# Kernel tuning notes

Measured on AMD Instinct MI355X. Metric: run time of the kernel, lower is better.

Reference implementation:

```python
import jax, jax.numpy as jnp
import numpy as np

N = [100000, 25000, 6250]        # nodes per scale (coarsening pyramid)
F = 128                          # features_per_scale (all equal)
H = 4                            # num_heads (only enters via the score scale)
SCALE = float((F // H) ** 0.5)
OUT = 5                          # out_channels
E_SAME = [1000000, 400000, 100000]
E_INC = [400000, 100000]


def _cross_attn(src, dst, src_feat, n_dst, qW, qb, kW, kb, vW, vb):
    # GAT-style gather -> per-edge score -> segment softmax over dst -> scatter.
    # In the original model dst_feat is zeros, so Q = 0 @ qW + qb; we keep the
    # matmul so qW appears in the autodiff graph (its grad is zero, faithfully).
    K = src_feat @ kW + kb
    V = src_feat @ vW + vb
    Q = jnp.zeros((n_dst, qW.shape[1]), src_feat.dtype) @ qW + qb
    score = (Q[dst] * K[src]).sum(-1) / SCALE            # [E]
    m = jax.ops.segment_max(score, dst, num_segments=n_dst)
    e = jnp.exp(score - m[dst])
    denom = jax.ops.segment_sum(e, dst, num_segments=n_dst)
    attn = e / denom[dst]                                # segment softmax
    return jax.ops.segment_sum(attn[:, None] * V[src], dst, num_segments=n_dst)


def _gcn(src, dst, x, n, W, b):
    # DGL GraphConv, norm='both': D_out^-1/2 -> scatter-sum -> D_in^-1/2 -> linear.
    ones = jnp.ones(src.shape[0], x.dtype)
    deg_out = jnp.clip(jax.ops.segment_sum(ones, src, num_segments=n), 1.0)
    deg_in = jnp.clip(jax.ops.segment_sum(ones, dst, num_segments=n), 1.0)
    h = x * jax.lax.rsqrt(deg_out)[:, None]
    agg = jax.ops.segment_sum(h[src], dst, num_segments=n)
    return (agg * jax.lax.rsqrt(deg_in)[:, None]) @ W + b


def setup_inputs() -> dict:
    key = jax.random.key(0)
    cnt = [0]
    def rkey():
        cnt[0] += 1
        return jax.random.fold_in(key, cnt[0])
    def rn(shape, s=0.05):
        return jax.random.normal(rkey(), shape, jnp.float32) * s
    def ri(n, hi):
        return jax.random.randint(rkey(), (n,), 0, hi, jnp.int32)
    return {
        "X": rn((N[0], F), 1.0),
        "emb_W": rn((F, F)), "emb_b": rn((F,)),
        "gcn_W": rn((3, F, F)), "gcn_b": rn((3, F)),
        "enc_qW": rn((2, F, F)), "enc_qb": rn((2, F)),
        "enc_kW": rn((2, F, F)), "enc_kb": rn((2, F)),
        "enc_vW": rn((2, F, F)), "enc_vb": rn((2, F)),
        "dec_qW": rn((2, F, F)), "dec_qb": rn((2, F)),
        "dec_kW": rn((2, F, F)), "dec_kb": rn((2, F)),
        "dec_vW": rn((2, F, F)), "dec_vb": rn((2, F)),
        "head_W": rn((3, 2 * F, OUT)), "head_b": rn((3, OUT)),
        "g0_src": ri(E_SAME[0], N[0]), "g0_dst": ri(E_SAME[0], N[0]),
        "g1_src": ri(E_SAME[1], N[1]), "g1_dst": ri(E_SAME[1], N[1]),
        "g2_src": ri(E_SAME[2], N[2]), "g2_dst": ri(E_SAME[2], N[2]),
        "inc0_src": ri(E_INC[0], N[0]), "inc0_dst": ri(E_INC[0], N[1]),
        "inc1_src": ri(E_INC[1], N[1]), "inc1_dst": ri(E_INC[1], N[2]),
        "dec0_src": ri(E_INC[1], N[2]), "dec0_dst": ri(E_INC[1], N[1]),
        "dec1_src": ri(E_INC[0], N[1]), "dec1_dst": ri(E_INC[0], N[0]),
    }


def reference(X, emb_W, emb_b, gcn_W, gcn_b,
              enc_qW, enc_qb, enc_kW, enc_kb, enc_vW, enc_vb,
              dec_qW, dec_qb, dec_kW, dec_kb, dec_vW, dec_vb,
              head_W, head_b,
              g0_src, g0_dst, g1_src, g1_dst, g2_src, g2_dst,
              inc0_src, inc0_dst, inc1_src, inc1_dst,
              dec0_src, dec0_dst, dec1_src, dec1_dst):
    h0 = X @ emb_W + emb_b                               # embedding, scale 0
    # encoder: scale 0 -> 1 -> 2
    e1 = _cross_attn(inc0_src, inc0_dst, h0, N[1],
                     enc_qW[0], enc_qb[0], enc_kW[0], enc_kb[0], enc_vW[0], enc_vb[0])
    e2 = _cross_attn(inc1_src, inc1_dst, e1, N[2],
                     enc_qW[1], enc_qb[1], enc_kW[1], enc_kb[1], enc_vW[1], enc_vb[1])
    feats = [h0, e1, e2]
    edges = [(g0_src, g0_dst), (g1_src, g1_dst), (g2_src, g2_dst)]
    gcn_out = [_gcn(s, d, feats[i], N[i], gcn_W[i], gcn_b[i])
               for i, (s, d) in enumerate(edges)]
    # decoder: scale 2 -> 1 -> 0
    d1 = _cross_attn(dec0_src, dec0_dst, gcn_out[2], N[1],
                     dec_qW[0], dec_qb[0], dec_kW[0], dec_kb[0], dec_vW[0], dec_vb[0])
    d0 = _cross_attn(dec1_src, dec1_dst, d1, N[0],
                     dec_qW[1], dec_qb[1], dec_kW[1], dec_kb[1], dec_vW[1], dec_vb[1])
    decoded = [d0, d1, gcn_out[2]]
    outs = [jax.nn.softmax(jnp.concatenate([gcn_out[i], decoded[i]], -1) @ head_W[i] + head_b[i], -1)
            for i in range(3)]
    return jnp.concatenate(outs, 0)                      # [N0+N1+N2, OUT]
```

## Files before the change

### kernel.cpp

```cpp
#include <hip/hip_runtime.h>
#include <math.h>

#define N0 100000
#define N1 25000
#define N2 6250
#define FD 128

typedef unsigned short u16;
typedef unsigned int u32;

static inline int ceildiv(int a, int b){ return (a + b - 1)/b; }

__device__ __forceinline__ u16 f2bf(float f){
  u32 u = __float_as_uint(f);
  u += 0x7fffu + ((u >> 16) & 1u);
  return (u16)(u >> 16);
}
__device__ __forceinline__ float bf2f(u16 h){
  return __uint_as_float(((u32)h) << 16);
}
__device__ __forceinline__ float blo(u32 u){ return __uint_as_float(u << 16); }
__device__ __forceinline__ float bhi(u32 u){ return __uint_as_float(u & 0xffff0000u); }
__device__ __forceinline__ u32 pk2(float a, float b){ return (u32)f2bf(a) | ((u32)f2bf(b) << 16); }

struct BMeta {
  const int* key[10];
  const int* src[7];
  int* rowp[7]; int* csr[7];
  float* rsout[3];
  int n[10], E[10], B[10], r[10];
  int eoff[8];
  int soff[4];
  int boff[11];
  int pblk[11];
};

__device__ __forceinline__ void mm_inner(const float* Al, const float* Wl, int r0, int c0, float acc[4][4]){
  #pragma unroll
  for (int kq = 0; kq < 8; ++kq) {
    int k0 = kq*4;
    float4 a[4], w[4];
    #pragma unroll
    for (int i=0;i<4;++i) a[i] = *(const float4*)&Al[(r0+i)*32 + k0];
    #pragma unroll
    for (int kk=0;kk<4;++kk) w[kk] = *(const float4*)&Wl[(k0+kk)*128 + c0];
    #pragma unroll
    for (int i=0;i<4;++i){
      acc[i][0] = fmaf(a[i].x,w[0].x, fmaf(a[i].y,w[1].x, fmaf(a[i].z,w[2].x, fmaf(a[i].w,w[3].x, acc[i][0]))));
      acc[i][1] = fmaf(a[i].x,w[0].y, fmaf(a[i].y,w[1].y, fmaf(a[i].z,w[2].y, fmaf(a[i].w,w[3].y, acc[i][1]))));
      acc[i][2] = fmaf(a[i].x,w[0].z, fmaf(a[i].y,w[1].z, fmaf(a[i].z,w[2].z, fmaf(a[i].w,w[3].z, acc[i][2]))));
      acc[i][3] = fmaf(a[i].x,w[0].w, fmaf(a[i].y,w[1].w, fmaf(a[i].z,w[2].w, fmaf(a[i].w,w[3].w, acc[i][3]))));
    }
  }
}

template<int SCORE, int AB16>
__device__ __forceinline__ void dev_gemm(float* Wl, float* Al, int bid,
    const void* __restrict__ Ap,
    const float* __restrict__ W, const float* __restrict__ bias,
    const float* __restrict__ kvec, float* __restrict__ sOut,
    u16* __restrict__ out, int n)
{
  const int tid = threadIdx.x;
  const int row0 = bid * 32;
  const int c0 = (tid & 31) * 4, r0 = (tid >> 5) * 4;
  const int r = tid >> 3, fc = tid & 7;
  const int gr_s = row0 + r;
  float acc[4][4] = {};
  float sacc = 0.f;
  const float4* W4 = (const float4*)W;
  for (int kp = 0; kp < 4; ++kp) {
    float4* Wl4 = (float4*)Wl;
    #pragma unroll
    for (int i = 0; i < 4; ++i) Wl4[tid + 256*i] = W4[kp*1024 + tid + 256*i];
    {
      float4 v = make_float4(0.f,0.f,0.f,0.f);
      if (gr_s < n){
        if (AB16){
          ushort4 h = ((const ushort4*)Ap)[(size_t)gr_s*32 + kp*8 + fc];
          v = make_float4(bf2f(h.x), bf2f(h.y), bf2f(h.z), bf2f(h.w));
        } else {
          v = ((const float4*)Ap)[(size_t)gr_s*32 + kp*8 + fc];
        }
      }
      ((float4*)Al)[tid] = v;
      if (SCORE){
        float4 kv = *(const float4*)&kvec[kp*32 + fc*4];
        sacc += v.x*kv.x + v.y*kv.y + v.z*kv.z + v.w*kv.w;
      }
    }
    __syncthreads();
    mm_inner(Al, Wl, r0, c0, acc);
    __syncthreads();
  }
  if (SCORE){
    sacc += __shfl_xor(sacc, 1);
    sacc += __shfl_xor(sacc, 2);
    sacc += __shfl_xor(sacc, 4);
    if (fc == 0 && gr_s < n) sOut[gr_s] = expf(sacc + kvec[128]);
  }
  float4 bv = make_float4(0.f,0.f,0.f,0.f);
  if (bias) bv = *(const float4*)&bias[c0];
  #pragma unroll
  for (int i=0;i<4;++i){
    int gr = row0 + r0 + i;
    if (gr < n){
      ushort4 o;
      o.x = f2bf(acc[i][0]+bv.x); o.y = f2bf(acc[i][1]+bv.y);
      o.z = f2bf(acc[i][2]+bv.z); o.w = f2bf(acc[i][3]+bv.w);
      *(ushort4*)&out[(size_t)gr*FD + c0] = o;
    }
  }
}

template<int AB16>
__device__ __forceinline__ void dev_dualgemm(float* sm, int bid,
    const void* __restrict__ Ap,
    const float* __restrict__ Wv, const float* __restrict__ vb,
    const float* __restrict__ Wg,
    const float* __restrict__ kvec, float* __restrict__ sOut,
    u16* __restrict__ Vout, u16* __restrict__ Yout, int n)
{
  float* WvL = sm; float* WgL = sm + 4096; float* Al = sm + 8192;
  const int tid = threadIdx.x;
  const int row0 = bid * 32;
  const int c0 = (tid & 31) * 4, r0 = (tid >> 5) * 4;
  const int r = tid >> 3, fc = tid & 7;
  const int gr_s = row0 + r;
  float accV[4][4] = {};
  float accY[4][4] = {};
  float sacc = 0.f;
  const float4* Wv4 = (const float4*)Wv;
  const float4* Wg4 = (const float4*)Wg;
  for (int kp = 0; kp < 4; ++kp) {
    #pragma unroll
    for (int i = 0; i < 4; ++i) ((float4*)WvL)[tid + 256*i] = Wv4[kp*1024 + tid + 256*i];
    #pragma unroll
    for (int i = 0; i < 4; ++i) ((float4*)WgL)[tid + 256*i] = Wg4[kp*1024 + tid + 256*i];
    {
      float4 v = make_float4(0.f,0.f,0.f,0.f);
      if (gr_s < n){
        if (AB16){
          ushort4 h = ((const ushort4*)Ap)[(size_t)gr_s*32 + kp*8 + fc];
          v = make_float4(bf2f(h.x), bf2f(h.y), bf2f(h.z), bf2f(h.w));
        } else {
          v = ((const float4*)Ap)[(size_t)gr_s*32 + kp*8 + fc];
        }
      }
      ((float4*)Al)[tid] = v;
      float4 kv = *(const float4*)&kvec[kp*32 + fc*4];
      sacc += v.x*kv.x + v.y*kv.y + v.z*kv.z + v.w*kv.w;
    }
    __syncthreads();
    mm_inner(Al, WvL, r0, c0, accV);
    mm_inner(Al, WgL, r0, c0, accY);
    __syncthreads();
  }
  sacc += __shfl_xor(sacc, 1);
  sacc += __shfl_xor(sacc, 2);
  sacc += __shfl_xor(sacc, 4);
  if (fc == 0 && gr_s < n) sOut[gr_s] = expf(sacc + kvec[128]);
  float4 bv = *(const float4*)&vb[c0];
  #pragma unroll
  for (int i=0;i<4;++i){
    int gr = row0 + r0 + i;
    if (gr < n){
      ushort4 o;
      o.x = f2bf(accV[i][0]+bv.x); o.y = f2bf(accV[i][1]+bv.y);
      o.z = f2bf(accV[i][2]+bv.z); o.w = f2bf(accV[i][3]+bv.w);
      *(ushort4*)&Vout[(size_t)gr*FD + c0] = o;
      ushort4 y;
      y.x = f2bf(accY[i][0]); y.y = f2bf(accY[i][1]);
      y.z = f2bf(accY[i][2]); y.w = f2bf(accY[i][3]);
      *(ushort4*)&Yout[(size_t)gr*FD + c0] = y;
    }
  }
}

__device__ __forceinline__ int job_of_blk(const BMeta& m, int bid){
  int j = 0;
  #pragma unroll
  for (int t = 1; t < 10; ++t) if (bid >= m.pblk[t]) j = t;
  return j;
}

__device__ __forceinline__ void dev_p0(const BMeta& m, int bid, int* __restrict__ bktCnt, int* sh){
  int j = job_of_blk(m, bid);
  int lb = bid - m.pblk[j];
  const int* key = m.key[j]; int E = m.E[j], r = m.r[j], B = m.B[j];
  if (threadIdx.x < 64) sh[threadIdx.x] = 0;
  __syncthreads();
  int base = lb*4096 + threadIdx.x;
  #pragma unroll
  for (int i = 0; i < 16; ++i){ int e = base + i*256; if (e < E) atomicAdd(&sh[key[e]/r], 1); }
  __syncthreads();
  if ((int)threadIdx.x < B) atomicAdd(&bktCnt[m.boff[j] + threadIdx.x], sh[threadIdx.x]);
}

__device__ __forceinline__ void dev_p1(const BMeta& m, const int* __restrict__ bktCnt,
    int* __restrict__ bktBase, int* __restrict__ bktCur, int* sh){
  int tid = threadIdx.x;
  for (int i = tid; i < 328; i += 256) sh[i] = bktCnt[i];
  __syncthreads();
  if (tid < 10){
    int acc = (tid < 7) ? m.eoff[tid] : m.soff[tid-7];
    for (int b = m.boff[tid]; b < m.boff[tid+1]; ++b){ int v = sh[b]; sh[b] = acc; acc += v; }
  }
  __syncthreads();
  for (int i = tid; i < 328; i += 256){ bktBase[i] = sh[i]; bktCur[i] = sh[i]; }
}

__device__ __forceinline__ void dev_p2(const BMeta& m, int bid, int* __restrict__ bktCur,
    u32* __restrict__ ebuf, u16* __restrict__ ebuf16, int* sh){
  int j = job_of_blk(m, bid);
  int lb = bid - m.pblk[j];
  const int* key = m.key[j];
  int E = m.E[j], r = m.r[j], B = m.B[j];
  int* h = sh; int* start = sh + 64;
  if (threadIdx.x < 64) h[threadIdx.x] = 0;
  __syncthreads();
  int base = lb*4096 + threadIdx.x;
  #pragma unroll
  for (int i = 0; i < 16; ++i){ int e = base + i*256; if (e < E) atomicAdd(&h[key[e]/r], 1); }
  __syncthreads();
  if ((int)threadIdx.x < B) start[threadIdx.x] = atomicAdd(&bktCur[m.boff[j] + threadIdx.x], h[threadIdx.x]);
  __syncthreads();
  if (j < 7){
    const int* src = m.src[j];
    #pragma unroll
    for (int i = 0; i < 16; ++i){
      int e = base + i*256;
      if (e < E){
        int s = src[e], d = key[e];
        int b = d / r;
        int pos = atomicAdd(&start[b], 1);
        ebuf[pos] = ((u32)(d - b*r) << 17) | (u32)s;
      }
    }
  } else {
    #pragma unroll
    for (int i = 0; i < 16; ++i){
      int e = base + i*256;
      if (e < E){
        int k = key[e];
        int b = k / r;
        int pos = atomicAdd(&start[b], 1);
        ebuf16[pos] = (u16)(k - b*r);
      }
    }
  }
}

__device__ __forceinline__ void dev_p3(const BMeta& m, int bb,
    const int* __restrict__ bktCnt, const int* __restrict__ bktBase,
    const u32* __restrict__ ebuf, const u16* __restrict__ ebuf16, int* sh){
  int j = 0;
  #pragma unroll
  for (int t = 1; t < 10; ++t) if (bb >= m.boff[t]) j = t;
  int b = bb - m.boff[j];
  int n = m.n[j], r = m.r[j];
  int node0 = b*r;
  int rr = min(r, n - node0);
  int gbase = bktBase[bb];
  int cnt = bktCnt[bb];
  int tid = threadIdx.x;
  if (j >= 7){
    int* hist = sh;
    for (int i = tid; i < rr; i += 256) hist[i] = 0;
    __syncthreads();
    for (int e = tid; e < cnt; e += 256) atomicAdd(&hist[ebuf16[gbase + e]], 1);
    __syncthreads();
    float* rs = m.rsout[j-7];
    for (int i = tid; i < rr; i += 256) rs[node0 + i] = rsqrtf(fmaxf((float)hist[i], 1.f));
    return;
  }
  int B = m.B[j];
  int* rowp = m.rowp[j]; int* csr = m.csr[j];
  int lbase = gbase - m.eoff[j];
  int* hist = sh; int* aux = sh + 1568;
  for (int i = tid; i < rr; i += 256) hist[i] = 0;
  __syncthreads();
  for (int e = tid; e < cnt; e += 256){ u32 pk = ebuf[gbase + e]; atomicAdd(&hist[pk >> 17], 1); }
  __syncthreads();
  int ch = (rr + 255) >> 8;
  int i0 = tid*ch;
  int s = 0;
  for (int k = 0; k < ch; ++k){ int idx = i0 + k; if (idx < rr){ int t = hist[idx]; hist[idx] = s; s += t; } }
  aux[tid] = s; __syncthreads();
  for (int off = 1; off < 256; off <<= 1){
    int v = aux[tid]; int a = (tid >= off) ? aux[tid - off] : 0;
    __syncthreads();
    aux[tid] = v + a;
    __syncthreads();
  }
  int pre = (tid ? aux[tid-1] : 0) + lbase;
  for (int k = 0; k < ch; ++k){ int idx = i0 + k; if (idx < rr) hist[idx] += pre; }
  __syncthreads();
  for (int i = tid; i < rr; i += 256) rowp[node0 + i] = hist[i];
  if (b == B-1 && tid == 0) rowp[n] = lbase + cnt;
  __syncthreads();
  for (int e = tid; e < cnt; e += 256){
    u32 pk = ebuf[gbase + e];
    int pos = atomicAdd(&hist[pk >> 17], 1);
    csr[pos] = (int)(pk & 0x1FFFFu);
  }
}

template<int OB16>
__device__ __forceinline__ void dev_attn_gather16(int bid,
    const int* __restrict__ csr, const int* __restrict__ rowp,
    const float* __restrict__ w, const u16* __restrict__ V,
    void* __restrict__ out, int n)
{
  int g = threadIdx.x >> 4, lane = threadIdx.x & 15;
  int row = bid*16 + g;
  if (row >= n) return;
  int st = rowp[row], en = rowp[row+1];
  float a0=0,a1=0,a2=0,a3=0,a4=0,a5=0,a6=0,a7=0;
  if (en > st){
    const uint4* V8 = (const uint4*)V;
    float den = 0.f;
    for (int e = st; e < en; ++e){
      int sn = csr[e];
      float x = w[sn];
      uint4 v = V8[(size_t)sn*16 + lane];
      den += x;
      a0 = fmaf(x, blo(v.x), a0); a1 = fmaf(x, bhi(v.x), a1);
      a2 = fmaf(x, blo(v.y), a2); a3 = fmaf(x, bhi(v.y), a3);
      a4 = fmaf(x, blo(v.z), a4); a5 = fmaf(x, bhi(v.z), a5);
      a6 = fmaf(x, blo(v.w), a6); a7 = fmaf(x, bhi(v.w), a7);
    }
    float inv = 1.f/den;
    a0*=inv; a1*=inv; a2*=inv; a3*=inv; a4*=inv; a5*=inv; a6*=inv; a7*=inv;
  }
  if (OB16){
    uint4 o; o.x = pk2(a0,a1); o.y = pk2(a2,a3); o.z = pk2(a4,a5); o.w = pk2(a6,a7);
    ((uint4*)out)[(size_t)row*16 + lane] = o;
  } else {
    float4* o4 = (float4*)out;
    o4[(size_t)row*32 + lane*2]     = make_float4(a0,a1,a2,a3);
    o4[(size_t)row*32 + lane*2 + 1] = make_float4(a4,a5,a6,a7);
  }
}

template<int OB16>
__device__ __forceinline__ void dev_gcn_gather16(int bid,
    const int* __restrict__ csr, const int* __restrict__ rowp,
    const float* __restrict__ rs, const u16* __restrict__ Y,
    const float* __restrict__ bias, void* __restrict__ out, int n)
{
  int g = threadIdx.x >> 4, lane = threadIdx.x & 15;
  int row = bid*16 + g;
  if (row >= n) return;
  int st = rowp[row], en = rowp[row+1];
  float a0=0,a1=0,a2=0,a3=0,a4=0,a5=0,a6=0,a7=0;
  const uint4* Y8 = (const uint4*)Y;
  for (int e = st; e < en; ++e){
    int sn = csr[e];
    float x = rs[sn];
    uint4 v = Y8[(size_t)sn*16 + lane];
    a0 = fmaf(x, blo(v.x), a0); a1 = fmaf(x, bhi(v.x), a1);
    a2 = fmaf(x, blo(v.y), a2); a3 = fmaf(x, bhi(v.y), a3);
    a4 = fmaf(x, blo(v.z), a4); a5 = fmaf(x, bhi(v.z), a5);
    a6 = fmaf(x, blo(v.w), a6); a7 = fmaf(x, bhi(v.w), a7);
  }
  float sc = rsqrtf(fmaxf((float)(en - st), 1.f));
  const float4* b4 = (const float4*)bias;
  float4 ba = b4[lane*2], bb = b4[lane*2+1];
  float o0=fmaf(a0,sc,ba.x), o1=fmaf(a1,sc,ba.y), o2=fmaf(a2,sc,ba.z), o3=fmaf(a3,sc,ba.w);
  float o4v=fmaf(a4,sc,bb.x), o5=fmaf(a5,sc,bb.y), o6=fmaf(a6,sc,bb.z), o7=fmaf(a7,sc,bb.w);
  if (OB16){
    uint4 o; o.x = pk2(o0,o1); o.y = pk2(o2,o3); o.z = pk2(o4v,o5); o.w = pk2(o6,o7);
    ((uint4*)out)[(size_t)row*16 + lane] = o;
  } else {
    float4* o4 = (float4*)out;
    o4[(size_t)row*32 + lane*2]     = make_float4(o0,o1,o2,o3);
    o4[(size_t)row*32 + lane*2 + 1] = make_float4(o4v,o5,o6,o7);
  }
}

template<int GB16, int DB16>
__device__ __forceinline__ void dev_head(int bid, const void* __restrict__ g, const void* __restrict__ dch,
    const float* __restrict__ W, const float* __restrict__ b,
    float* __restrict__ out, int n, int rowOff)
{
  int wid = threadIdx.x >> 6, lane = threadIdx.x & 63;
  int row = bid*4 + wid;
  if (row >= n) return;
  float x0, x1, x2, x3;
  if (GB16){ const u16* gr = (const u16*)g + (size_t)row*FD; x0 = bf2f(gr[lane]); x1 = bf2f(gr[64+lane]); }
  else     { const float* gr = (const float*)g + (size_t)row*FD; x0 = gr[lane]; x1 = gr[64+lane]; }
  if (DB16){ const u16* dr = (const u16*)dch + (size_t)row*FD; x2 = bf2f(dr[lane]); x3 = bf2f(dr[64+lane]); }
  else     { const float* dr = (const float*)dch + (size_t)row*FD; x2 = dr[lane]; x3 = dr[64+lane]; }
  float acc[5];
  #pragma unroll
  for (int o = 0; o < 5; ++o)
    acc[o] = x0*W[lane*5+o] + x1*W[(64+lane)*5+o] + x2*W[(128+lane)*5+o] + x3*W[(192+lane)*5+o];
  #pragma unroll
  for (int o = 0; o < 5; ++o)
    #pragma unroll
    for (int s = 32; s; s >>= 1) acc[o] += __shfl_xor(acc[o], s);
  if (lane == 0){
    float m = -1e30f;
    #pragma unroll
    for (int o = 0; o < 5; ++o){ acc[o] += b[o]; m = fmaxf(m, acc[o]); }
    float sum = 0.f;
    #pragma unroll
    for (int o = 0; o < 5; ++o){ acc[o] = expf(acc[o]-m); sum += acc[o]; }
    float is = 1.0f/sum;
    float* op = out + (size_t)(rowOff+row)*5;
    #pragma unroll
    for (int o = 0; o < 5; ++o) op[o] = acc[o]*is;
  }
}


__global__ __launch_bounds__(256) void k1_zero_kqv(int* __restrict__ zeroBlk, int ntot,
    const float* __restrict__ ekW, const float* __restrict__ ekb, const float* __restrict__ eqb,
    const float* __restrict__ dkW, const float* __restrict__ dkb, const float* __restrict__ dqb,
    float* __restrict__ kv, float inv)
{
  int bid = blockIdx.x;
  if (bid < 4){
    if (threadIdx.x < 128){
      int j = bid;
      const float* kW = (j < 2) ? ekW + j*16384 : dkW + (j-2)*16384;
      const float* kb = (j < 2) ? ekb + j*128   : dkb + (j-2)*128;
      const float* qb = (j < 2) ? eqb + j*128   : dqb + (j-2)*128;
      float* o = kv + j*132;
      int k = threadIdx.x;
      float a = 0.f;
      for (int t = 0; t < 128; ++t) a = fmaf(kW[k*128+t], qb[t], a);
      o[k] = a * inv;
      if (k == 0){
        float c = 0.f;
        for (int t = 0; t < 128; ++t) c = fmaf(kb[t], qb[t], c);
        o[128] = c * inv;
      }
    }
  } else {
    int i = (bid-4)*256 + threadIdx.x;
    if (i < ntot) zeroBlk[i] = 0;
  }
}

__global__ __launch_bounds__(256) void k2_p0_gemm(BMeta m, int* __restrict__ bktCnt,
    const float* __restrict__ X, const float* __restrict__ W, const float* __restrict__ b,
    u16* __restrict__ bh0, int np0)
{
  __shared__ float sm[5120];
  int bid = blockIdx.x;
  if (bid < np0) dev_p0(m, bid, bktCnt, (int*)sm);
  else dev_gemm<0,0>(sm, sm+4096, bid - np0, X, W, b, nullptr, nullptr, bh0, N0);
}

__global__ __launch_bounds__(256) void k3_p1(BMeta m,
    const int* __restrict__ bktCnt, int* __restrict__ bktBase, int* __restrict__ bktCur)
{
  __shared__ int sh[384];
  dev_p1(m, bktCnt, bktBase, bktCur, sh);
}

__global__ __launch_bounds__(256) void k4_p2_dual(BMeta m, int* __restrict__ bktCur,
    u32* __restrict__ ebuf, u16* __restrict__ ebuf16,
    const u16* __restrict__ bh0,
    const float* __restrict__ evW, const float* __restrict__ evb, const float* __restrict__ gW,
    const float* __restrict__ kvec, float* __restrict__ sS, u16* __restrict__ bV, u16* __restrict__ bY0,
    int np2, int gOff)
{
  __shared__ float sm[9216];
  int bid = blockIdx.x;
  if (bid < np2) dev_p2(m, bid, bktCur, ebuf, ebuf16, (int*)sm);
  else dev_dualgemm<1>(sm, gOff + bid - np2, bh0, evW, evb, gW, kvec, sS, bV, bY0, N0);
}

__global__ __launch_bounds__(256) void k5_p3_dual(BMeta m,
    const int* __restrict__ bktCnt, const int* __restrict__ bktBase,
    const u32* __restrict__ ebuf, const u16* __restrict__ ebuf16,
    const u16* __restrict__ bh0,
    const float* __restrict__ evW, const float* __restrict__ evb, const float* __restrict__ gW,
    const float* __restrict__ kvec, float* __restrict__ sS, u16* __restrict__ bV, u16* __restrict__ bY0,
    int np3, int gOff)
{
  __shared__ float sm[9216];
  int bid = blockIdx.x;
  if (bid < np3) dev_p3(m, bid, bktCnt, bktBase, ebuf, ebuf16, (int*)sm);
  else dev_dualgemm<1>(sm, gOff + bid - np3, bh0, evW, evb, gW, kvec, sS, bV, bY0, N0);
}

__global__ __launch_bounds__(256) void k6_ag_i0(
    const int* __restrict__ csrA, const int* __restrict__ rowpA,
    const float* __restrict__ sS, const u16* __restrict__ bV, u16* __restrict__ be1,
    const int* __restrict__ csr0, const int* __restrict__ rowp0, const float* __restrict__ rs0,
    const u16* __restrict__ bY0, const float* __restrict__ gb, u16* __restrict__ bg0, int nMain, int sBase)
{
  int bid = blockIdx.x;
  if (bid < nMain) dev_attn_gather16<1>(bid, csrA, rowpA, sS, bV, be1, N1);
  else dev_gcn_gather16<1>(sBase + bid - nMain, csr0, rowp0, rs0, bY0, gb, bg0, N0);
}

__global__ __launch_bounds__(256) void k7_dual_enc1(
    const u16* __restrict__ be1,
    const float* __restrict__ vW, const float* __restrict__ vb, const float* __restrict__ gW,
    const float* __restrict__ kvec, float* __restrict__ sS, u16* __restrict__ bV, u16* __restrict__ bY1,
    const int* __restrict__ csr0, const int* __restrict__ rowp0, const float* __restrict__ rs0,
    const u16* __restrict__ bY0, const float* __restrict__ gb, u16* __restrict__ bg0, int nMain, int sBase)
{
  __shared__ float sm[9216];
  int bid = blockIdx.x;
  if (bid < nMain) dev_dualgemm<1>(sm, bid, be1, vW, vb, gW, kvec, sS, bV, bY1, N1);
  else dev_gcn_gather16<1>(sBase + bid - nMain, csr0, rowp0, rs0, bY0, gb, bg0, N0);
}

__global__ __launch_bounds__(256) void k8_ag_i1(
    const int* __restrict__ csrA, const int* __restrict__ rowpA,
    const float* __restrict__ sS, const u16* __restrict__ bV, float* __restrict__ be2,
    const int* __restrict__ csr0, const int* __restrict__ rowp0, const float* __restrict__ rs0,
    const u16* __restrict__ bY0, const float* __restrict__ gb, u16* __restrict__ bg0, int nMain, int sBase)
{
  int bid = blockIdx.x;
  if (bid < nMain) dev_attn_gather16<0>(bid, csrA, rowpA, sS, bV, be2, N2);
  else dev_gcn_gather16<1>(sBase + bid - nMain, csr0, rowp0, rs0, bY0, gb, bg0, N0);
}

__global__ __launch_bounds__(256) void k9_y2_g1(
    const float* __restrict__ be2, const float* __restrict__ W2, u16* __restrict__ bY2,
    const int* __restrict__ csr1, const int* __restrict__ rowp1, const float* __restrict__ rs1,
    const u16* __restrict__ bY1, const float* __restrict__ b1, u16* __restrict__ bg1,
    const int* __restrict__ csr0, const int* __restrict__ rowp0, const float* __restrict__ rs0,
    const u16* __restrict__ bY0, const float* __restrict__ gb, u16* __restrict__ bg0,
    int ngemm, int nMain, int sBase)
{
  __shared__ float sm[5120];
  int bid = blockIdx.x;
  if (bid < ngemm) dev_gemm<0,0>(sm, sm+4096, bid, be2, W2, nullptr, nullptr, nullptr, bY2, N2);
  else if (bid < nMain) dev_gcn_gather16<1>(bid - ngemm, csr1, rowp1, rs1, bY1, b1, bg1, N1);
  else dev_gcn_gather16<1>(sBase + bid - nMain, csr0, rowp0, rs0, bY0, gb, bg0, N0);
}

__global__ __launch_bounds__(256) void k10_g2(
    const int* __restrict__ csr2, const int* __restrict__ rowp2, const float* __restrict__ rs2,
    const u16* __restrict__ bY2, const float* __restrict__ b2, float* __restrict__ bg2,
    const int* __restrict__ csr0, const int* __restrict__ rowp0, const float* __restrict__ rs0,
    const u16* __restrict__ bY0, const float* __restrict__ gb, u16* __restrict__ bg0, int nMain, int sBase)
{
  int bid = blockIdx.x;
  if (bid < nMain) dev_gcn_gather16<0>(bid, csr2, rowp2, rs2, bY2, b2, bg2, N2);
  else dev_gcn_gather16<1>(sBase + bid - nMain, csr0, rowp0, rs0, bY0, gb, bg0, N0);
}

__global__ __launch_bounds__(256) void k11_dec0_head2(
    const float* __restrict__ bg2, const float* __restrict__ vW, const float* __restrict__ vb,
    const float* __restrict__ kvec, float* __restrict__ sS, u16* __restrict__ bV,
    const float* __restrict__ hW, const float* __restrict__ hb, float* __restrict__ out,
    const int* __restrict__ csr0, const int* __restrict__ rowp0, const float* __restrict__ rs0,
    const u16* __restrict__ bY0, const float* __restrict__ gb, u16* __restrict__ bg0,
    int ngemm, int nMain, int sBase)
{
  __shared__ float sm[5120];
  int bid = blockIdx.x;
  if (bid < ngemm) dev_gemm<1,0>(sm, sm+4096, bid, bg2, vW, vb, kvec, sS, bV, N2);
  else if (bid < nMain) dev_head<0,0>(bid - ngemm, bg2, bg2, hW, hb, out, N2, N0+N1);
  else dev_gcn_gather16<1>(sBase + bid - nMain, csr0, rowp0, rs0, bY0, gb, bg0, N0);
}

__global__ __launch_bounds__(256) void k12_ag_d1(
    const int* __restrict__ csrA, const int* __restrict__ rowpA,
    const float* __restrict__ sS, const u16* __restrict__ bV, u16* __restrict__ be1,
    const int* __restrict__ csr0, const int* __restrict__ rowp0, const float* __restrict__ rs0,
    const u16* __restrict__ bY0, const float* __restrict__ gb, u16* __restrict__ bg0, int nMain, int sBase)
{
  int bid = blockIdx.x;
  if (bid < nMain) dev_attn_gather16<1>(bid, csrA, rowpA, sS, bV, be1, N1);
  else dev_gcn_gather16<1>(sBase + bid - nMain, csr0, rowp0, rs0, bY0, gb, bg0, N0);
}

__global__ __launch_bounds__(256) void k13_dec1_head1(
    const u16* __restrict__ be1, const float* __restrict__ vW, const float* __restrict__ vb,
    const float* __restrict__ kvec, float* __restrict__ sS, u16* __restrict__ bV,
    const u16* __restrict__ bg1, const float* __restrict__ hW, const float* __restrict__ hb,
    float* __restrict__ out,
    const int* __restrict__ csr0, const int* __restrict__ rowp0, const float* __restrict__ rs0,
    const u16* __restrict__ bY0, const float* __restrict__ gb, u16* __restrict__ bg0,
    int ngemm, int nMain, int sBase)
{
  __shared__ float sm[5120];
  int bid = blockIdx.x;
  if (bid < ngemm) dev_gemm<1,1>(sm, sm+4096, bid, be1, vW, vb, kvec, sS, bV, N1);
  else if (bid < nMain) dev_head<1,1>(bid - ngemm, bg1, be1, hW, hb, out, N1, N0);
  else dev_gcn_gather16<1>(sBase + bid - nMain, csr0, rowp0, rs0, bY0, gb, bg0, N0);
}

__global__ __launch_bounds__(256) void k14_gather_head0(
    const int* __restrict__ csr, const int* __restrict__ rowp,
    const float* __restrict__ w, const u16* __restrict__ V,
    const u16* __restrict__ bg0,
    const float* __restrict__ hW, const float* __restrict__ hb,
    float* __restrict__ out)
{
  int g = threadIdx.x >> 4, lane = threadIdx.x & 15;
  int row = blockIdx.x*16 + g;
  if (row >= N0) return;
  int st = rowp[row], en = rowp[row+1];
  float a0=0,a1=0,a2=0,a3=0,a4=0,a5=0,a6=0,a7=0;
  if (en > st){
    const uint4* V8 = (const uint4*)V;
    float den = 0.f;
    for (int e = st; e < en; ++e){
      int sn = csr[e];
      float x = w[sn];
      uint4 v = V8[(size_t)sn*16 + lane];
      den += x;
      a0 = fmaf(x, blo(v.x), a0); a1 = fmaf(x, bhi(v.x), a1);
      a2 = fmaf(x, blo(v.y), a2); a3 = fmaf(x, bhi(v.y), a3);
      a4 = fmaf(x, blo(v.z), a4); a5 = fmaf(x, bhi(v.z), a5);
      a6 = fmaf(x, blo(v.w), a6); a7 = fmaf(x, bhi(v.w), a7);
    }
    float inv = 1.f/den;
    a0*=inv; a1*=inv; a2*=inv; a3*=inv; a4*=inv; a5*=inv; a6*=inv; a7*=inv;
  }
  uint4 gv = ((const uint4*)(bg0 + (size_t)row*FD))[lane];
  float g0 = blo(gv.x), g1 = bhi(gv.x), g2 = blo(gv.y), g3 = bhi(gv.y);
  float g4 = blo(gv.z), g5 = bhi(gv.z), g6 = blo(gv.w), g7 = bhi(gv.w);
  int j = 8*lane;
  float acc[5];
  #pragma unroll
  for (int o = 0; o < 5; ++o){
    acc[o] = g0*hW[(j+0)*5+o] + g1*hW[(j+1)*5+o] + g2*hW[(j+2)*5+o] + g3*hW[(j+3)*5+o]
           + g4*hW[(j+4)*5+o] + g5*hW[(j+5)*5+o] + g6*hW[(j+6)*5+o] + g7*hW[(j+7)*5+o]
           + a0*hW[(128+j+0)*5+o] + a1*hW[(128+j+1)*5+o] + a2*hW[(128+j+2)*5+o] + a3*hW[(128+j+3)*5+o]
           + a4*hW[(128+j+4)*5+o] + a5*hW[(128+j+5)*5+o] + a6*hW[(128+j+6)*5+o] + a7*hW[(128+j+7)*5+o];
  }
  #pragma unroll
  for (int o = 0; o < 5; ++o)
    #pragma unroll
    for (int s = 8; s; s >>= 1) acc[o] += __shfl_xor(acc[o], s, 16);
  if (lane == 0){
    float m = -1e30f;
    #pragma unroll
    for (int o = 0; o < 5; ++o){ acc[o] += hb[o]; m = fmaxf(m, acc[o]); }
    float sum = 0.f;
    #pragma unroll
    for (int o = 0; o < 5; ++o){ acc[o] = expf(acc[o]-m); sum += acc[o]; }
    float is = 1.0f/sum;
    float* op = out + (size_t)row*5;
    #pragma unroll
    for (int o = 0; o < 5; ++o) op[o] = acc[o]*is;
  }
}

extern "C" void kernel_launch(void* const* d_in, const int* in_sizes, int n_in,
                              void* d_out, int out_size, void* d_ws, size_t ws_size,
                              hipStream_t stream)
{
  const float* X      = (const float*)d_in[0];
  const float* emb_W  = (const float*)d_in[1];
  const float* emb_b  = (const float*)d_in[2];
  const float* gcn_W  = (const float*)d_in[3];
  const float* gcn_b  = (const float*)d_in[4];
  const float* enc_qb = (const float*)d_in[6];
  const float* enc_kW = (const float*)d_in[7];
  const float* enc_kb = (const float*)d_in[8];
  const float* enc_vW = (const float*)d_in[9];
  const float* enc_vb = (const float*)d_in[10];
  const float* dec_qb = (const float*)d_in[12];
  const float* dec_kW = (const float*)d_in[13];
  const float* dec_kb = (const float*)d_in[14];
  const float* dec_vW = (const float*)d_in[15];
  const float* dec_vb = (const float*)d_in[16];
  const float* head_W = (const float*)d_in[17];
  const float* head_b = (const float*)d_in[18];
  const int* g0s  = (const int*)d_in[19];
  const int* g0d  = (const int*)d_in[20];
  const int* g1s  = (const int*)d_in[21];
  const int* g1d  = (const int*)d_in[22];
  const int* g2s  = (const int*)d_in[23];
  const int* g2d  = (const int*)d_in[24];
  const int* i0s  = (const int*)d_in[25];
  const int* i0d  = (const int*)d_in[26];
  const int* i1s  = (const int*)d_in[27];
  const int* i1d  = (const int*)d_in[28];
  const int* dc0s = (const int*)d_in[29];
  const int* dc0d = (const int*)d_in[30];
  const int* dc1s = (const int*)d_in[31];
  const int* dc1d = (const int*)d_in[32];

  float* ws = (float*)d_ws;
  float* sS  = ws;
  float* kvec = sS + N0;
  float* be2 = kvec + 4*132;
  float* bg2 = be2 + (size_t)N2*FD;
  float* rs0 = bg2 + (size_t)N2*FD;
  float* rs1 = rs0 + N0;
  float* rs2 = rs1 + N1;
  u16*  bh0 = (u16*)(rs2 + N2 + 2);
  u16*  be1 = bh0 + (size_t)N0*FD;
  u16*  bg0 = be1 + (size_t)N1*FD;
  u16*  bg1 = bg0 + (size_t)N0*FD;
  u16*  bV  = bg1 + (size_t)N1*FD;
  u16*  bY0 = bV  + (size_t)N0*FD;
  u16*  bY1 = bV + 4000000;
  u16*  bY2 = bV + 8000000;
  int*  bktCnt  = (int*)(bY0 + (size_t)N0*FD);
  int*  bktBase = bktCnt + 328;
  int*  bktCur  = bktBase + 328;
  int*  rowpBlk = bktCur + 328;
  int*  csrBlk  = rowpBlk + 287507;
  u32*  ebuf    = (u32*)(csrBlk + 2500000);
  u16*  ebuf16  = (u16*)(ebuf + 2500000);

  const int* keyP[10] = {g0d,g1d,g2d,i0d,i1d,dc0d,dc1d, g0s,g1s,g2s};
  const int* srcP[7]  = {g0s,g1s,g2s,i0s,i1s,dc0s,dc1s};
  const int nArr[10] = {N0,N1,N2,N1,N2,N1,N0, N0,N1,N2};
  const int EArr[10] = {1000000,400000,100000,400000,100000,100000,400000, 1000000,400000,100000};
  const int BArr[10] = {64,32,8,32,8,16,64, 64,32,8};
  const int rArr[10] = {1563,782,782,782,782,1563,1563, 1563,782,782};

  BMeta m;
  {
    int eo=0, so=0, bo=0, po=0, ro=0, co=0;
    for (int j=0;j<10;++j){
      m.key[j]=keyP[j];
      m.n[j]=nArr[j]; m.E[j]=EArr[j]; m.B[j]=BArr[j]; m.r[j]=rArr[j];
      m.boff[j]=bo; m.pblk[j]=po;
      bo+=BArr[j]; po+=ceildiv(EArr[j],4096);
      if (j < 7){
        m.src[j]=srcP[j]; m.rowp[j]=rowpBlk+ro; m.csr[j]=csrBlk+co;
        m.eoff[j]=eo; eo+=EArr[j]; ro+=nArr[j]+1; co+=EArr[j];
      } else {
        m.soff[j-7]=so; so+=EArr[j];
      }
    }
    m.eoff[7]=eo; m.soff[3]=so; m.boff[10]=bo; m.pblk[10]=po;
  }
  m.rsout[0]=rs0; m.rsout[1]=rs1; m.rsout[2]=rs2;

  const float invScale = 0.17677669529663687f;
  float* out = (float*)d_out;

  const int NP = m.pblk[10];
  const int NB = m.boff[10];
  const int GH0 = ceildiv(N0,32);
  const int GH1 = ceildiv(N1,32);
  const int GH2 = ceildiv(N2,32);
  const int GS1 = 1250;
  const int GA1_16 = ceildiv(N1,16);
  const int GA2_16 = ceildiv(N2,16);
  const int G0B16  = ceildiv(N0,16);
  const int GH2H = ceildiv(N2,4);
  const int GH1H = ceildiv(N1,4);

  int ss[9];
  for (int i = 0; i <= 8; ++i) ss[i] = (int)(((long long)G0B16 * i) / 8);

  k1_zero_kqv<<<4 + ceildiv(NB,256), 256, 0, stream>>>(bktCnt, NB,
      enc_kW, enc_kb, enc_qb, dec_kW, dec_kb, dec_qb, kvec, invScale);
  k2_p0_gemm<<<NP + GH0, 256, 0, stream>>>(m, bktCnt, X, emb_W, emb_b, bh0, NP);
  k3_p1<<<1, 256, 0, stream>>>(m, bktCnt, bktBase, bktCur);
  k4_p2_dual<<<NP + GS1, 256, 0, stream>>>(m, bktCur, ebuf, ebuf16,
      bh0, enc_vW, enc_vb, gcn_W, kvec, sS, bV, bY0, NP, 0);
  k5_p3_dual<<<NB + (GH0 - GS1), 256, 0, stream>>>(m, bktCnt, bktBase, ebuf, ebuf16,
      bh0, enc_vW, enc_vb, gcn_W, kvec, sS, bV, bY0, NB, GS1);
  k6_ag_i0<<<GA1_16 + (ss[1]-ss[0]), 256, 0, stream>>>(m.csr[3], m.rowp[3], sS, bV, be1,
      m.csr[0], m.rowp[0], rs0, bY0, gcn_b, bg0, GA1_16, ss[0]);
  k7_dual_enc1<<<GH1 + (ss[2]-ss[1]), 256, 0, stream>>>(be1,
      enc_vW+16384, enc_vb+128, gcn_W+16384, kvec+132, sS, bV, bY1,
      m.csr[0], m.rowp[0], rs0, bY0, gcn_b, bg0, GH1, ss[1]);
  k8_ag_i1<<<GA2_16 + (ss[3]-ss[2]), 256, 0, stream>>>(m.csr[4], m.rowp[4], sS, bV, be2,
      m.csr[0], m.rowp[0], rs0, bY0, gcn_b, bg0, GA2_16, ss[2]);
  k9_y2_g1<<<GH2 + GA1_16 + (ss[4]-ss[3]), 256, 0, stream>>>(be2, gcn_W+32768, bY2,
      m.csr[1], m.rowp[1], rs1, bY1, gcn_b+128, bg1,
      m.csr[0], m.rowp[0], rs0, bY0, gcn_b, bg0, GH2, GH2+GA1_16, ss[3]);
  k10_g2<<<GA2_16 + (ss[5]-ss[4]), 256, 0, stream>>>(m.csr[2], m.rowp[2], rs2, bY2, gcn_b+256, bg2,
      m.csr[0], m.rowp[0], rs0, bY0, gcn_b, bg0, GA2_16, ss[4]);
  k11_dec0_head2<<<GH2 + GH2H + (ss[6]-ss[5]), 256, 0, stream>>>(bg2, dec_vW, dec_vb, kvec+264, sS, bV,
      head_W+2560, head_b+10, out,
      m.csr[0], m.rowp[0], rs0, bY0, gcn_b, bg0, GH2, GH2+GH2H, ss[5]);
  k12_ag_d1<<<GA1_16 + (ss[7]-ss[6]), 256, 0, stream>>>(m.csr[5], m.rowp[5], sS, bV, be1,
      m.csr[0], m.rowp[0], rs0, bY0, gcn_b, bg0, GA1_16, ss[6]);
  k13_dec1_head1<<<GH1 + GH1H + (ss[8]-ss[7]), 256, 0, stream>>>(be1, dec_vW+16384, dec_vb+128, kvec+396, sS, bV,
      bg1, head_W+1280, head_b+5, out,
      m.csr[0], m.rowp[0], rs0, bY0, gcn_b, bg0, GH1, GH1+GH1H, ss[7]);
  k14_gather_head0<<<G0B16, 256, 0, stream>>>(m.csr[6], m.rowp[6], sS, bV, bg0,
      head_W, head_b, out);
}
```

Before: 457.1 us.

## Use bf16 MFMA for the dual V/GCN projection GEMMs with pre-transposed weights

Replaces the shared-memory FP32 dual GEMM (V projection plus GCN weight product) with a 16x16x32 bf16 MFMA version that reads activations and pre-transposed bf16 weights straight from global memory. A prep kernel now also converts and transposes the encoder V and GCN weights to bf16. The GEMM block split between the two overlapped kernels is also shifted. The intent is to cut FP32 ALU time and LDS traffic in these GEMMs. The cost is bf16 rounding of the weights and uncoalesced 2-byte scattered output stores.

```diff
diff --git a/kernel.cpp b/kernel.cpp
--- a/kernel.cpp
+++ b/kernel.cpp
@@ -1,5 +1,6 @@
 #include <hip/hip_runtime.h>
 #include <math.h>
+#include <stdint.h>
 
 #define N0 100000
 #define N1 25000
@@ -8,6 +9,8 @@
 
 typedef unsigned short u16;
 typedef unsigned int u32;
+typedef short bf16x8 __attribute__((ext_vector_type(8)));
+typedef float f32x4 __attribute__((ext_vector_type(4)));
 
 static inline int ceildiv(int a, int b){ return (a + b - 1)/b; }
 
@@ -113,66 +116,57 @@
   }
 }
 
-template<int AB16>
-__device__ __forceinline__ void dev_dualgemm(float* sm, int bid,
-    const void* __restrict__ Ap,
-    const float* __restrict__ Wv, const float* __restrict__ vb,
-    const float* __restrict__ Wg,
-    const float* __restrict__ kvec, float* __restrict__ sOut,
+__device__ __forceinline__ void dev_dual_mfma(int bid,
+    const u16* __restrict__ A, const u16* __restrict__ WvT, const u16* __restrict__ WgT,
+    const float* __restrict__ vb, const float* __restrict__ kvec, float* __restrict__ sOut,
     u16* __restrict__ Vout, u16* __restrict__ Yout, int n)
 {
-  float* WvL = sm; float* WgL = sm + 4096; float* Al = sm + 8192;
   const int tid = threadIdx.x;
+  const int wid = tid >> 6, lane = tid & 63;
+  const int l15 = lane & 15, lg = lane >> 4;
+  const int rt = wid & 1;
+  const int cbase = (wid >> 1) * 64;
   const int row0 = bid * 32;
-  const int c0 = (tid & 31) * 4, r0 = (tid >> 5) * 4;
-  const int r = tid >> 3, fc = tid & 7;
-  const int gr_s = row0 + r;
-  float accV[4][4] = {};
-  float accY[4][4] = {};
+  const int arow = row0 + rt*16 + l15;
+  const int arowc = min(arow, n-1);
+  f32x4 accV[4] = {{0.f,0.f,0.f,0.f},{0.f,0.f,0.f,0.f},{0.f,0.f,0.f,0.f},{0.f,0.f,0.f,0.f}};
+  f32x4 accY[4] = {{0.f,0.f,0.f,0.f},{0.f,0.f,0.f,0.f},{0.f,0.f,0.f,0.f},{0.f,0.f,0.f,0.f}};
   float sacc = 0.f;
-  const float4* Wv4 = (const float4*)Wv;
-  const float4* Wg4 = (const float4*)Wg;
-  for (int kp = 0; kp < 4; ++kp) {
-    #pragma unroll
-    for (int i = 0; i < 4; ++i) ((float4*)WvL)[tid + 256*i] = Wv4[kp*1024 + tid + 256*i];
-    #pragma unroll
-    for (int i = 0; i < 4; ++i) ((float4*)WgL)[tid + 256*i] = Wg4[kp*1024 + tid + 256*i];
-    {
-      float4 v = make_float4(0.f,0.f,0.f,0.f);
-      if (gr_s < n){
-        if (AB16){
-          ushort4 h = ((const ushort4*)Ap)[(size_t)gr_s*32 + kp*8 + fc];
-          v = make_float4(bf2f(h.x), bf2f(h.y), bf2f(h.z), bf2f(h.w));
-        } else {
-          v = ((const float4*)Ap)[(size_t)gr_s*32 + kp*8 + fc];
-        }
+  #pragma unroll
+  for (int ks = 0; ks < 4; ++ks){
+    const int ko = ks*32 + lg*8;
+    bf16x8 a = *(const bf16x8*)(A + (size_t)arowc*FD + ko);
+    if (wid < 2){
+      float4 k0 = *(const float4*)(kvec + ko);
+      float4 k1 = *(const float4*)(kvec + ko + 4);
+      sacc += bf2f((u16)a[0])*k0.x + bf2f((u16)a[1])*k0.y + bf2f((u16)a[2])*k0.z + bf2f((u16)a[3])*k0.w
+            + bf2f((u16)a[4])*k1.x + bf2f((u16)a[5])*k1.y + bf2f((u16)a[6])*k1.z + bf2f((u16)a[7])*k1.w;
+    }
+    #pragma unroll
+    for (int ct = 0; ct < 4; ++ct){
+      const int col = cbase + ct*16 + l15;
+      bf16x8 bv = *(const bf16x8*)(WvT + (size_t)col*FD + ko);
+      bf16x8 bg = *(const bf16x8*)(WgT + (size_t)col*FD + ko);
+      accV[ct] = __builtin_amdgcn_mfma_f32_16x16x32_bf16(a, bv, accV[ct], 0, 0, 0);
+      accY[ct] = __builtin_amdgcn_mfma_f32_16x16x32_bf16(a, bg, accY[ct], 0, 0, 0);
+    }
+  }
+  if (wid < 2){
+    sacc += __shfl_xor(sacc, 16);
+    sacc += __shfl_xor(sacc, 32);
+    if (lane < 16 && arow < n) sOut[arow] = expf(sacc + kvec[128]);
+  }
+  #pragma unroll
+  for (int ct = 0; ct < 4; ++ct){
+    const int col = cbase + ct*16 + l15;
+    const float bvv = vb[col];
+    #pragma unroll
+    for (int i = 0; i < 4; ++i){
+      int gr = row0 + rt*16 + lg*4 + i;
+      if (gr < n){
+        Vout[(size_t)gr*FD + col] = f2bf(accV[ct][i] + bvv);
+        Yout[(size_t)gr*FD + col] = f2bf(accY[ct][i]);
       }
-      ((float4*)Al)[tid] = v;
-      float4 kv = *(const float4*)&kvec[kp*32 + fc*4];
-      sacc += v.x*kv.x + v.y*kv.y + v.z*kv.z + v.w*kv.w;
-    }
-    __syncthreads();
-    mm_inner(Al, WvL, r0, c0, accV);
-    mm_inner(Al, WgL, r0, c0, accY);
-    __syncthreads();
-  }
-  sacc += __shfl_xor(sacc, 1);
-  sacc += __shfl_xor(sacc, 2);
-  sacc += __shfl_xor(sacc, 4);
-  if (fc == 0 && gr_s < n) sOut[gr_s] = expf(sacc + kvec[128]);
-  float4 bv = *(const float4*)&vb[c0];
-  #pragma unroll
-  for (int i=0;i<4;++i){
-    int gr = row0 + r0 + i;
-    if (gr < n){
-      ushort4 o;
-      o.x = f2bf(accV[i][0]+bv.x); o.y = f2bf(accV[i][1]+bv.y);
-      o.z = f2bf(accV[i][2]+bv.z); o.w = f2bf(accV[i][3]+bv.w);
-      *(ushort4*)&Vout[(size_t)gr*FD + c0] = o;
-      ushort4 y;
-      y.x = f2bf(accY[i][0]); y.y = f2bf(accY[i][1]);
-      y.z = f2bf(accY[i][2]); y.w = f2bf(accY[i][3]);
-      *(ushort4*)&Yout[(size_t)gr*FD + c0] = y;
     }
   }
 }
@@ -415,10 +409,12 @@
 }
 
 
-__global__ __launch_bounds__(256) void k1_zero_kqv(int* __restrict__ zeroBlk, int ntot,
+__global__ __launch_bounds__(256) void k1_prep(int* __restrict__ zeroBlk, int ntot,
     const float* __restrict__ ekW, const float* __restrict__ ekb, const float* __restrict__ eqb,
     const float* __restrict__ dkW, const float* __restrict__ dkb, const float* __restrict__ dqb,
-    float* __restrict__ kv, float inv)
+    float* __restrict__ kv, float inv,
+    const float* __restrict__ evW, const float* __restrict__ gW,
+    u16* __restrict__ wvt0, u16* __restrict__ wgt0, u16* __restrict__ wvt1, u16* __restrict__ wgt1)
 {
   int bid = blockIdx.x;
   if (bid < 4){
@@ -438,8 +434,18 @@
         o[128] = c * inv;
       }
     }
+  } else if (bid < 8){
+    const float* Ws; u16* Wd;
+    if (bid == 4){ Ws = evW;          Wd = wvt0; }
+    else if (bid == 5){ Ws = gW;      Wd = wgt0; }
+    else if (bid == 6){ Ws = evW+16384; Wd = wvt1; }
+    else { Ws = gW+16384; Wd = wgt1; }
+    for (int i = threadIdx.x; i < 16384; i += 256){
+      int k = i >> 7, c = i & 127;
+      Wd[c*128 + k] = f2bf(Ws[i]);
+    }
   } else {
-    int i = (bid-4)*256 + threadIdx.x;
+    int i = (bid-8)*256 + threadIdx.x;
     if (i < ntot) zeroBlk[i] = 0;
   }
 }
@@ -464,28 +470,28 @@
 __global__ __launch_bounds__(256) void k4_p2_dual(BMeta m, int* __restrict__ bktCur,
     u32* __restrict__ ebuf, u16* __restrict__ ebuf16,
     const u16* __restrict__ bh0,
-    const float* __restrict__ evW, const float* __restrict__ evb, const float* __restrict__ gW,
+    const u16* __restrict__ wvt0, const u16* __restrict__ wgt0, const float* __restrict__ evb,
     const float* __restrict__ kvec, float* __restrict__ sS, u16* __restrict__ bV, u16* __restrict__ bY0,
     int np2, int gOff)
 {
-  __shared__ float sm[9216];
-  int bid = blockIdx.x;
-  if (bid < np2) dev_p2(m, bid, bktCur, ebuf, ebuf16, (int*)sm);
-  else dev_dualgemm<1>(sm, gOff + bid - np2, bh0, evW, evb, gW, kvec, sS, bV, bY0, N0);
+  __shared__ int sh[1824];
+  int bid = blockIdx.x;
+  if (bid < np2) dev_p2(m, bid, bktCur, ebuf, ebuf16, sh);
+  else dev_dual_mfma(gOff + bid - np2, bh0, wvt0, wgt0, evb, kvec, sS, bV, bY0, N0);
 }
 
 __global__ __launch_bounds__(256) void k5_p3_dual(BMeta m,
     const int* __restrict__ bktCnt, const int* __restrict__ bktBase,
     const u32* __restrict__ ebuf, const u16* __restrict__ ebuf16,
     const u16* __restrict__ bh0,
-    const float* __restrict__ evW, const float* __restrict__ evb, const float* __restrict__ gW,
+    const u16* __restrict__ wvt0, const u16* __restrict__ wgt0, const float* __restrict__ evb,
     const float* __restrict__ kvec, float* __restrict__ sS, u16* __restrict__ bV, u16* __restrict__ bY0,
     int np3, int gOff)
 {
-  __shared__ float sm[9216];
-  int bid = blockIdx.x;
-  if (bid < np3) dev_p3(m, bid, bktCnt, bktBase, ebuf, ebuf16, (int*)sm);
-  else dev_dualgemm<1>(sm, gOff + bid - np3, bh0, evW, evb, gW, kvec, sS, bV, bY0, N0);
+  __shared__ int sh[1824];
+  int bid = blockIdx.x;
+  if (bid < np3) dev_p3(m, bid, bktCnt, bktBase, ebuf, ebuf16, sh);
+  else dev_dual_mfma(gOff + bid - np3, bh0, wvt0, wgt0, evb, kvec, sS, bV, bY0, N0);
 }
 
 __global__ __launch_bounds__(256) void k6_ag_i0(
@@ -501,14 +507,13 @@
 
 __global__ __launch_bounds__(256) void k7_dual_enc1(
     const u16* __restrict__ be1,
-    const float* __restrict__ vW, const float* __restrict__ vb, const float* __restrict__ gW,
+    const u16* __restrict__ wvt1, const u16* __restrict__ wgt1, const float* __restrict__ vb,
     const float* __restrict__ kvec, float* __restrict__ sS, u16* __restrict__ bV, u16* __restrict__ bY1,
     const int* __restrict__ csr0, const int* __restrict__ rowp0, const float* __restrict__ rs0,
     const u16* __restrict__ bY0, const float* __restrict__ gb, u16* __restrict__ bg0, int nMain, int sBase)
 {
-  __shared__ float sm[9216];
-  int bid = blockIdx.x;
-  if (bid < nMain) dev_dualgemm<1>(sm, bid, be1, vW, vb, gW, kvec, sS, bV, bY1, N1);
+  int bid = blockIdx.x;
+  if (bid < nMain) dev_dual_mfma(bid, be1, wvt1, wgt1, vb, kvec, sS, bV, bY1, N1);
   else dev_gcn_gather16<1>(sBase + bid - nMain, csr0, rowp0, rs0, bY0, gb, bg0, N0);
 }
 
@@ -708,6 +713,11 @@
   int*  csrBlk  = rowpBlk + 287507;
   u32*  ebuf    = (u32*)(csrBlk + 2500000);
   u16*  ebuf16  = (u16*)(ebuf + 2500000);
+  uintptr_t wtp = ((uintptr_t)(ebuf16 + 1500000) + 15) & ~(uintptr_t)15;
+  u16* wvt0 = (u16*)wtp;
+  u16* wgt0 = wvt0 + 16384;
+  u16* wvt1 = wgt0 + 16384;
+  u16* wgt1 = wvt1 + 16384;
 
   const int* keyP[10] = {g0d,g1d,g2d,i0d,i1d,dc0d,dc1d, g0s,g1s,g2s};
   const int* srcP[7]  = {g0s,g1s,g2s,i0s,i1s,dc0s,dc1s};
@@ -743,7 +753,7 @@
   const int GH0 = ceildiv(N0,32);
   const int GH1 = ceildiv(N1,32);
   const int GH2 = ceildiv(N2,32);
-  const int GS1 = 1250;
+  const int GS1 = 1563;
   const int GA1_16 = ceildiv(N1,16);
   const int GA2_16 = ceildiv(N2,16);
   const int G0B16  = ceildiv(N0,16);
@@ -753,18 +763,19 @@
   int ss[9];
   for (int i = 0; i <= 8; ++i) ss[i] = (int)(((long long)G0B16 * i) / 8);
 
-  k1_zero_kqv<<<4 + ceildiv(NB,256), 256, 0, stream>>>(bktCnt, NB,
-      enc_kW, enc_kb, enc_qb, dec_kW, dec_kb, dec_qb, kvec, invScale);
+  k1_prep<<<8 + ceildiv(NB,256), 256, 0, stream>>>(bktCnt, NB,
+      enc_kW, enc_kb, enc_qb, dec_kW, dec_kb, dec_qb, kvec, invScale,
+      enc_vW, gcn_W, wvt0, wgt0, wvt1, wgt1);
   k2_p0_gemm<<<NP + GH0, 256, 0, stream>>>(m, bktCnt, X, emb_W, emb_b, bh0, NP);
   k3_p1<<<1, 256, 0, stream>>>(m, bktCnt, bktBase, bktCur);
   k4_p2_dual<<<NP + GS1, 256, 0, stream>>>(m, bktCur, ebuf, ebuf16,
-      bh0, enc_vW, enc_vb, gcn_W, kvec, sS, bV, bY0, NP, 0);
+      bh0, wvt0, wgt0, enc_vb, kvec, sS, bV, bY0, NP, 0);
   k5_p3_dual<<<NB + (GH0 - GS1), 256, 0, stream>>>(m, bktCnt, bktBase, ebuf, ebuf16,
-      bh0, enc_vW, enc_vb, gcn_W, kvec, sS, bV, bY0, NB, GS1);
+      bh0, wvt0, wgt0, enc_vb, kvec, sS, bV, bY0, NB, GS1);
   k6_ag_i0<<<GA1_16 + (ss[1]-ss[0]), 256, 0, stream>>>(m.csr[3], m.rowp[3], sS, bV, be1,
       m.csr[0], m.rowp[0], rs0, bY0, gcn_b, bg0, GA1_16, ss[0]);
   k7_dual_enc1<<<GH1 + (ss[2]-ss[1]), 256, 0, stream>>>(be1,
-      enc_vW+16384, enc_vb+128, gcn_W+16384, kvec+132, sS, bV, bY1,
+      wvt1, wgt1, enc_vb+128, kvec+132, sS, bV, bY1,
       m.csr[0], m.rowp[0], rs0, bY0, gcn_b, bg0, GH1, ss[1]);
   k8_ag_i1<<<GA2_16 + (ss[3]-ss[2]), 256, 0, stream>>>(m.csr[4], m.rowp[4], sS, bV, be2,
       m.csr[0], m.rowp[0], rs0, bY0, gcn_b, bg0, GA2_16, ss[2]);
```

Result: faster. 447.8 us (-2.0%).
